# Kernel tuning notes

Hardware: AMD Instinct MI355X
Metric: run time of the kernel (lower is better)

## Reference

```python
import jax, jax.numpy as jnp
import numpy as np

N, E, G = 100000, 1600000, 1000
D_IN, D, L, C = 128, 300, 5, 10


def setup_inputs() -> dict:
    key = jax.random.key(0)
    ks = jax.random.split(key, 32)
    s = 0.05
    inp = {
        'x': jax.random.normal(ks[0], (N, D_IN), jnp.float32),
        'edge_index': jax.random.randint(ks[1], (2, E), 0, N, jnp.int64),
        'batch': jnp.sort(jax.random.randint(ks[2], (N,), 0, G, jnp.int64)),
        'enc_W': jax.random.normal(ks[3], (D_IN, D)) * s,
        'enc_b': jnp.zeros((D,)),
        'eps': jnp.zeros((L,)),
        'cW1': jax.random.normal(ks[4], (L, D, 2 * D)) * s,
        'cb1': jnp.zeros((L, 2 * D)),
        'cbn_s': jnp.ones((L, 2 * D)),
        'cbn_b': jnp.zeros((L, 2 * D)),
        'cW2': jax.random.normal(ks[5], (L, 2 * D, D)) * s,
        'cb2': jnp.zeros((L, D)),
        'bn_s': jnp.ones((L, D)),
        'bn_b': jnp.zeros((L, D)),
        'vn0': jnp.zeros((D,)),
        'vW1': jax.random.normal(ks[6], (L, D, 2 * D)) * s,
        'vb1': jnp.zeros((L, 2 * D)),
        'vbn1_s': jnp.ones((L, 2 * D)),
        'vbn1_b': jnp.zeros((L, 2 * D)),
        'vW2': jax.random.normal(ks[7], (L, 2 * D, D)) * s,
        'vb2': jnp.zeros((L, D)),
        'vbn2_s': jnp.ones((L, D)),
        'vbn2_b': jnp.zeros((L, D)),
        'gW1': jax.random.normal(ks[8], (D, 2 * D)) * s,
        'gb1': jnp.zeros((2 * D,)),
        'gbn_s': jnp.ones((2 * D,)),
        'gbn_b': jnp.zeros((2 * D,)),
        'gW2': jax.random.normal(ks[9], (2 * D, 1)) * s,
        'gb2': jnp.zeros((1,)),
        'pW': jax.random.normal(ks[10], (D, C)) * s,
        'pb': jnp.zeros((C,)),
    }
    return inp


def reference(x, enc_W, enc_b, eps, cW1, cb1, cbn_s, cbn_b, cW2, cb2,
              bn_s, bn_b, vn0, vW1, vb1, vbn1_s, vbn1_b, vW2, vb2,
              vbn2_s, vbn2_b, gW1, gb1, gbn_s, gbn_b, gW2, gb2, pW, pb,
              edge_index, batch):
    src, dst = edge_index[0], edge_index[1]
    n = x.shape[0]
    vn = jnp.broadcast_to(vn0, (G, D))  # virtualnode_embedding(zeros) -> row 0 per graph
    h_list = [x @ enc_W + enc_b]
    for l in range(L):
        hl = h_list[l] + vn[batch]  # virtual-node broadcast gather
        # GIN conv: MLP((1+eps)*h + sum_{j in N(i)} h_j)
        agg = jax.ops.segment_sum(hl[src], dst, num_segments=n)
        t = (1.0 + eps[l]) * hl + agg
        t = jax.nn.relu((t @ cW1[l] + cb1[l]) * cbn_s[l] + cbn_b[l])
        h = (t @ cW2[l] + cb2[l]) * bn_s[l] + bn_b[l]  # layer BN (eval, folded)
        if l < L - 1:
            h = jax.nn.relu(h)  # dropout is identity in eval
        # virtual-node update: global_add_pool + MLP
        vtmp = jax.ops.segment_sum(hl, batch, num_segments=G) + vn
        u = jax.nn.relu((vtmp @ vW1[l] + vb1[l]) * vbn1_s[l] + vbn1_b[l])
        vn = jax.nn.relu((u @ vW2[l] + vb2[l]) * vbn2_s[l] + vbn2_b[l])
        h_list.append(h)
    # JK = 'max' across all L+1 layer outputs
    nr = jnp.max(jnp.stack(h_list, axis=0), axis=0)  # [N, D]
    # GlobalAttention pooling: gate_nn -> per-graph segment softmax
    gate = (jax.nn.relu((nr @ gW1 + gb1) * gbn_s + gbn_b) @ gW2 + gb2)[:, 0]
    gmax = jax.ops.segment_max(gate, batch, num_segments=G)
    e = jnp.exp(gate - gmax[batch])
    denom = jax.ops.segment_sum(e, batch, num_segments=G)
    alpha = e / denom[batch]
    graph_rep = jax.ops.segment_sum(nr * alpha[:, None], batch, num_segments=G)
    return graph_rep @ pW + pb  # [G, C]
```

## Files before the change

### kernel.cpp

```cpp
#include <hip/hip_runtime.h>
#include <cstddef>

#define NGRAPH 1000
#define NEDGES 1600000
#define DD     300
#define DD2    600
#define DIN    128
#define NLAYER 5
#define NCLS   10
#define BR     32
#define BRM    32

#define NT2 38
#define NK2 10
#define NT3 19
#define NK3 19
#define WFRAG 1024
#define W1F_SZ (NT2*NK2*WFRAG)

typedef unsigned short u16;
typedef unsigned char  u8;
typedef unsigned int   u32;
typedef __attribute__((ext_vector_type(8))) short short8;
typedef __attribute__((ext_vector_type(4))) short short4v;
typedef __attribute__((ext_vector_type(4))) float f32x4;

__device__ __forceinline__ u16 f2bf(float f) {
    u32 u; __builtin_memcpy(&u, &f, 4);
    u = (u + 0x7FFFu + ((u >> 16) & 1u)) >> 16;
    return (u16)u;
}
__device__ __forceinline__ float bf2f(u16 h) {
    u32 u = ((u32)h) << 16;
    float f; __builtin_memcpy(&f, &u, 4); return f;
}

__device__ __forceinline__ float ld24(const u16* __restrict__ hi, const u8* __restrict__ lo,
                                      size_t idx) {
    u32 u = ((u32)hi[idx] << 16) | ((u32)lo[idx] << 8);
    float f; __builtin_memcpy(&f, &u, 4); return f;
}
__device__ __forceinline__ void st24(u16* __restrict__ hi, u8* __restrict__ lo,
                                     size_t idx, float f) {
    u32 u; __builtin_memcpy(&u, &f, 4);
    u32 r = u + 0x7Fu + ((u >> 8) & 1u);
    hi[idx] = (u16)(r >> 16); lo[idx] = (u8)(r >> 8);
}
__device__ __forceinline__ void ld24x4(const u16* __restrict__ hi, const u8* __restrict__ lo,
                                       size_t idx, float o[4]) {
    ushort4 h = *(const ushort4*)(hi + idx);
    uchar4  l = *(const uchar4*)(lo + idx);
    u32 u0 = ((u32)h.x << 16) | ((u32)l.x << 8);
    u32 u1 = ((u32)h.y << 16) | ((u32)l.y << 8);
    u32 u2 = ((u32)h.z << 16) | ((u32)l.z << 8);
    u32 u3 = ((u32)h.w << 16) | ((u32)l.w << 8);
    __builtin_memcpy(&o[0], &u0, 4); __builtin_memcpy(&o[1], &u1, 4);
    __builtin_memcpy(&o[2], &u2, 4); __builtin_memcpy(&o[3], &u3, 4);
}
__device__ __forceinline__ void st24x4(u16* __restrict__ hi, u8* __restrict__ lo,
                                       size_t idx, const float v[4]) {
    u32 u[4];
#pragma unroll
    for (int q = 0; q < 4; ++q) {
        u32 t; __builtin_memcpy(&t, &v[q], 4);
        u[q] = t + 0x7Fu + ((t >> 8) & 1u);
    }
    ushort4 h; h.x = (u16)(u[0] >> 16); h.y = (u16)(u[1] >> 16);
    h.z = (u16)(u[2] >> 16); h.w = (u16)(u[3] >> 16);
    uchar4 l8; l8.x = (u8)(u[0] >> 8); l8.y = (u8)(u[1] >> 8);
    l8.z = (u8)(u[2] >> 8); l8.w = (u8)(u[3] >> 8);
    *(ushort4*)(hi + idx) = h;
    *(uchar4*)(lo + idx) = l8;
}

__global__ void diag_kernel(float* __restrict__ out, int n, float val)
{
    int i = blockIdx.x * 256 + threadIdx.x;
    if (i < n) out[i] = val;
}

__global__ void vn_init_kernel(float* __restrict__ vn, const float* __restrict__ vn0)
{
    int idx = blockIdx.x * 256 + threadIdx.x;
    if (idx < NGRAPH * DD) vn[idx] = vn0[idx % DD];
}

__global__ void bconv_kernel(const int* __restrict__ braw, int n, int* __restrict__ b32)
{
    int i = blockIdx.x * 256 + threadIdx.x;
    if (i >= n) return;
    int fs = (braw[n - 1] == 0) ? 2 : 1;
    b32[i] = braw[(size_t)i * fs];
}

__global__ void packW_kernel(const float* __restrict__ W, int K, int N,
                             int nT, int nK, short* __restrict__ dst)
{
    int idx = blockIdx.x * 256 + threadIdx.x;
    int total = nT * nK * 64;
    if (idx >= total) return;
    int lane = idx & 63;
    int tk = idx >> 6;
    int nn = (tk / nK) * 16 + (lane & 15);
    int k0 = (tk % nK) * 32 + (lane >> 4) * 8;
    short* o = dst + ((size_t)tk << 10) + lane * 8;
#pragma unroll
    for (int j = 0; j < 8; ++j) {
        float v = (nn < N && (k0 + j) < K) ? W[(size_t)(k0 + j) * N + nn] : 0.f;
        u16 h = f2bf(v);
        o[j] = (short)h;
        o[512 + j] = (short)f2bf(v - bf2f(h));
    }
}

__global__ void deg_kernel(const int* __restrict__ ei, int fe, int E, int* __restrict__ deg)
{
    int e = blockIdx.x * 256 + threadIdx.x;
    if (e < E) atomicAdd(&deg[ei[(size_t)fe * (E + e)]], 1);
}

__global__ void scan_kernel(const int* __restrict__ deg, int* __restrict__ row_ptr, int n)
{
    __shared__ int sd[1024];
    int t = threadIdx.x;
    int C = (n + 1023) >> 10;
    int i0 = t * C, i1 = i0 + C; if (i1 > n) i1 = n; if (i0 > n) i0 = n;
    int s = 0;
    for (int i = i0; i < i1; ++i) s += deg[i];
    sd[t] = s;
    __syncthreads();
    for (int o = 1; o < 1024; o <<= 1) {
        int x = (t >= o) ? sd[t - o] : 0;
        __syncthreads();
        sd[t] += x;
        __syncthreads();
    }
    int run = (t == 0) ? 0 : sd[t - 1];
    for (int i = i0; i < i1; ++i) { row_ptr[i] = run; run += deg[i]; }
    if (t == 1023) row_ptr[n] = sd[1023];
}

__global__ void scatter_kernel(const int* __restrict__ ei, int fe, int E,
                               int* __restrict__ cursor, int* __restrict__ col_idx)
{
    int e = blockIdx.x * 256 + threadIdx.x;
    if (e < E) {
        int d = ei[(size_t)fe * (E + e)];
        int s = ei[(size_t)fe * e];
        int p = atomicAdd(&cursor[d], 1);
        col_idx[p] = s;
    }
}

__device__ __forceinline__ int lower_bound_i(const int* __restrict__ arr, int n, int key)
{
    int lo = 0, hi = n;
    while (lo < hi) {
        int mid = (lo + hi) >> 1;
        if (arr[mid] < key) lo = mid + 1; else hi = mid;
    }
    return lo;
}

__global__ void vtmp_kernel(const u16* __restrict__ hi, const u8* __restrict__ lo,
                            const int* __restrict__ batch, const float* __restrict__ vn,
                            float* __restrict__ vtmp, int n)
{
    int g = blockIdx.x, t = threadIdx.x;
    int l0 = lower_bound_i(batch, n, g);
    int h0 = lower_bound_i(batch, n, g + 1);
    if (t >= DD) return;
    float a0 = 0.f, a1 = 0.f, a2 = 0.f, a3 = 0.f;
    int i = l0;
    for (; i + 3 < h0; i += 4) {
        a0 += ld24(hi, lo, (size_t)(i + 0) * DD + t);
        a1 += ld24(hi, lo, (size_t)(i + 1) * DD + t);
        a2 += ld24(hi, lo, (size_t)(i + 2) * DD + t);
        a3 += ld24(hi, lo, (size_t)(i + 3) * DD + t);
    }
    for (; i < h0; ++i) a0 += ld24(hi, lo, (size_t)i * DD + t);
    vtmp[(size_t)g * DD + t] = ((a0 + a1) + (a2 + a3)) + vn[(size_t)g * DD + t];
}

__global__ void vn_mlp_kernel(const float* __restrict__ vtmp,
                              const float* __restrict__ W1, const float* __restrict__ b1,
                              const float* __restrict__ s1, const float* __restrict__ sb1,
                              const float* __restrict__ W2, const float* __restrict__ b2,
                              const float* __restrict__ s2, const float* __restrict__ sb2,
                              float* __restrict__ vn)
{
    __shared__ float vt[DD];
    __shared__ float us[DD2];
    int g = blockIdx.x, t = threadIdx.x;
    if (t < DD) vt[t] = vtmp[(size_t)g * DD + t];
    __syncthreads();
    for (int j = t; j < DD2; j += 512) {
        float acc = 0.f;
        for (int k = 0; k < DD; ++k) acc = fmaf(vt[k], W1[(size_t)k * DD2 + j], acc);
        us[j] = fmaxf(fmaf(acc + b1[j], s1[j], sb1[j]), 0.f);
    }
    __syncthreads();
    for (int j = t; j < DD; j += 512) {
        float acc = 0.f;
        for (int k = 0; k < DD2; ++k) acc = fmaf(us[k], W2[(size_t)k * DD + j], acc);
        vn[(size_t)g * DD + j] = fmaxf(fmaf(acc + b2[j], s2[j], sb2[j]), 0.f);
    }
}

__global__ __launch_bounds__(1024)
void encoder_kernel(const float* __restrict__ x, const float* __restrict__ W,
                    const float* __restrict__ b,
                    u16* __restrict__ Ahi, u8* __restrict__ Alo,
                    short* __restrict__ NRm, float* __restrict__ NRscale, int n)
{
    __shared__ float xs[BR][DIN];
    __shared__ float wmax[16][8];
    __shared__ float rowS[BR];
    const int tid = threadIdx.x;
    const int base = blockIdx.x * BR;
    for (int idx = tid; idx < BR * DIN; idx += 1024) {
        int r = idx >> 7, c = idx & 127;
        int node = base + r;
        xs[r][c] = (node < n) ? x[(size_t)node * DIN + c] : 0.f;
    }
    __syncthreads();
    const int rq = tid >> 8, ct = tid & 255;
    const int wid = tid >> 6, lane = tid & 63;
    const int j0 = ct; const bool has1 = ct < (DD - 256); const int j1 = ct + 256;
    float acc[8][2] = {};
    for (int k = 0; k < DIN; ++k) {
        const float* wr = W + (size_t)k * DD;
        float w0 = wr[j0], w1 = has1 ? wr[j1] : 0.f;
#pragma unroll
        for (int i = 0; i < 8; ++i) {
            float a = xs[rq * 8 + i][k];
            acc[i][0] = fmaf(a, w0, acc[i][0]);
            acc[i][1] = fmaf(a, w1, acc[i][1]);
        }
    }
    float bb0 = b[j0], bb1 = has1 ? b[j1] : 0.f;
    float v0[8], v1[8], lm[8];
#pragma unroll
    for (int i = 0; i < 8; ++i) {
        v0[i] = acc[i][0] + bb0;
        v1[i] = has1 ? (acc[i][1] + bb1) : 0.f;
        lm[i] = fmaxf(fabsf(v0[i]), fabsf(v1[i]));
    }
#pragma unroll
    for (int o = 32; o > 0; o >>= 1)
#pragma unroll
        for (int i = 0; i < 8; ++i) lm[i] = fmaxf(lm[i], __shfl_xor(lm[i], o));
    if (lane == 0)
#pragma unroll
        for (int i = 0; i < 8; ++i) wmax[wid][i] = lm[i];
    __syncthreads();
    if (ct < 8) {
        int r = rq * 8 + ct;
        float m = fmaxf(fmaxf(wmax[4 * rq][ct], wmax[4 * rq + 1][ct]),
                        fmaxf(wmax[4 * rq + 2][ct], wmax[4 * rq + 3][ct]));
        float S = fmaxf(m, 1e-30f) / 32767.f;
        rowS[r] = S;
        if (base + r < n) NRscale[base + r] = S;
    }
    __syncthreads();
#pragma unroll
    for (int i = 0; i < 8; ++i) {
        int r = rq * 8 + i;
        int node = base + r;
        if (node >= n) continue;
        float S = rowS[r];
        size_t idx = (size_t)node * DD + j0;
        st24(Ahi, Alo, idx, v0[i]);
        NRm[idx] = (short)rintf(v0[i] / S);
        if (has1) {
            st24(Ahi, Alo, idx + 256, v1[i]);
            NRm[idx + 256] = (short)rintf(v1[i] / S);
        }
    }
}

__global__ __launch_bounds__(256)
void agg_kernel(const u16* __restrict__ Phi, const u8* __restrict__ Plo,
                u16* __restrict__ Qhi, u8* __restrict__ Qlo,
                const int* __restrict__ row_ptr, const int* __restrict__ col_idx,
                const float* __restrict__ eps, int l, int n)
{
    int node = blockIdx.x * 4 + (threadIdx.x >> 6);
    int lane = threadIdx.x & 63;
    if (node >= n) return;
    const float ep = 1.0f + eps[l];
    const bool two = (lane < 11);
    float a0[4] = {0.f, 0.f, 0.f, 0.f}, a1[4] = {0.f, 0.f, 0.f, 0.f};
    int e0 = row_ptr[node], e1 = row_ptr[node + 1];
    for (int e = e0; e < e1; ++e) {
        int src = col_idx[e];
        size_t rb = (size_t)src * DD;
        float v[4];
        ld24x4(Phi, Plo, rb + lane * 4, v);
        a0[0] += v[0]; a0[1] += v[1]; a0[2] += v[2]; a0[3] += v[3];
        if (two) {
            ld24x4(Phi, Plo, rb + 256 + lane * 4, v);
            a1[0] += v[0]; a1[1] += v[1]; a1[2] += v[2]; a1[3] += v[3];
        }
    }
    size_t ob = (size_t)node * DD;
    float v[4], o[4];
    ld24x4(Phi, Plo, ob + lane * 4, v);
#pragma unroll
    for (int q = 0; q < 4; ++q) o[q] = fmaf(ep, v[q], a0[q]);
    st24x4(Qhi, Qlo, ob + lane * 4, o);
    if (two) {
        ld24x4(Phi, Plo, ob + 256 + lane * 4, v);
#pragma unroll
        for (int q = 0; q < 4; ++q) o[q] = fmaf(ep, v[q], a1[q]);
        st24x4(Qhi, Qlo, ob + 256 + lane * 4, o);
    }
}

__global__ __launch_bounds__(512)
void mlp_kernel(u16* __restrict__ Qhi, u8* __restrict__ Qlo,
                short* __restrict__ NRm, float* __restrict__ NRscale,
                const short* __restrict__ W1f, const float* __restrict__ b1,
                const float* __restrict__ s1, const float* __restrict__ sb1,
                const short* __restrict__ W2f, const float* __restrict__ b2,
                const float* __restrict__ s2, const float* __restrict__ sb2,
                int relu2, const float* __restrict__ vnp,
                const int* __restrict__ batch, int writeQ, int n)
{
    __shared__ char uni[78848];
    __shared__ float rowM[32], rowSo[32], rowSn[32];
    short* agh = (short*)uni;
    short* agl = (short*)(uni + 20992);
    short* tlh = (short*)uni;
    short* tll = (short*)(uni + 39424);
    float* outb = (float*)uni;

    const int tid = threadIdx.x;
    const int base = blockIdx.x * BRM;
    const int wv = tid >> 6, lane = tid & 63;
    const int cl = lane & 15, kq = lane >> 4, r0 = kq * 4;

    for (int idx = tid; idx < 32 * 80; idx += 512) {
        int r = idx / 80, c4 = (idx - r * 80) * 4;
        int node = base + r;
        float v[4] = {0.f, 0.f, 0.f, 0.f};
        if (c4 < DD && node < n) ld24x4(Qhi, Qlo, (size_t)node * DD + c4, v);
        short4v hh, ll;
#pragma unroll
        for (int q = 0; q < 4; ++q) {
            u16 h = f2bf(v[q]);
            hh[q] = (short)h;
            ll[q] = (short)f2bf(v[q] - bf2f(h));
        }
        *(short4v*)&agh[r * 328 + c4] = hh;
        *(short4v*)&agl[r * 328 + c4] = ll;
    }
    __syncthreads();

    {
        f32x4 acc[2][5];
#pragma unroll
        for (int s = 0; s < 2; ++s)
#pragma unroll
            for (int i = 0; i < 5; ++i) acc[s][i] = (f32x4){0.f, 0.f, 0.f, 0.f};
        const bool act5 = (wv + 32) < NT2;
        for (int ks = 0; ks < NK2; ++ks) {
            short8 bh[5], bl[5];
#pragma unroll
            for (int i = 0; i < 5; ++i) {
                int t = wv + 8 * i;
                if (i < 4 || act5) {
                    const short* bp = W1f + (((size_t)t * NK2 + ks) << 10) + lane * 8;
                    bh[i] = *(const short8*)bp;
                    bl[i] = *(const short8*)(bp + 512);
                }
            }
            short8 ah0 = *(const short8*)&agh[cl * 328 + kq * 8 + ks * 32];
            short8 al0 = *(const short8*)&agl[cl * 328 + kq * 8 + ks * 32];
            short8 ah1 = *(const short8*)&agh[(16 + cl) * 328 + kq * 8 + ks * 32];
            short8 al1 = *(const short8*)&agl[(16 + cl) * 328 + kq * 8 + ks * 32];
#pragma unroll
            for (int i = 0; i < 5; ++i)
                if (i < 4 || act5) {
                    acc[0][i] = __builtin_amdgcn_mfma_f32_16x16x32_bf16(ah0, bh[i], acc[0][i], 0, 0, 0);
                    acc[1][i] = __builtin_amdgcn_mfma_f32_16x16x32_bf16(ah1, bh[i], acc[1][i], 0, 0, 0);
                }
#pragma unroll
            for (int i = 0; i < 5; ++i)
                if (i < 4 || act5) {
                    acc[0][i] = __builtin_amdgcn_mfma_f32_16x16x32_bf16(ah0, bl[i], acc[0][i], 0, 0, 0);
                    acc[1][i] = __builtin_amdgcn_mfma_f32_16x16x32_bf16(ah1, bl[i], acc[1][i], 0, 0, 0);
                }
#pragma unroll
            for (int i = 0; i < 5; ++i)
                if (i < 4 || act5) {
                    acc[0][i] = __builtin_amdgcn_mfma_f32_16x16x32_bf16(al0, bh[i], acc[0][i], 0, 0, 0);
                    acc[1][i] = __builtin_amdgcn_mfma_f32_16x16x32_bf16(al1, bh[i], acc[1][i], 0, 0, 0);
                }
        }
        __syncthreads();
        if (tid < 256) {
            int r = tid >> 3, c = 600 + (tid & 7);
            tlh[r * 616 + c] = 0; tll[r * 616 + c] = 0;
        }
#pragma unroll
        for (int s = 0; s < 2; ++s)
#pragma unroll
            for (int i = 0; i < 5; ++i) {
                int t = wv + 8 * i;
                if (t >= NT2) continue;
                int cg = t * 16 + cl;
                if (cg < DD2) {
                    float bb = b1[cg], ss = s1[cg], cc = sb1[cg];
#pragma unroll
                    for (int r = 0; r < 4; ++r) {
                        float xv = fmaxf(fmaf(acc[s][i][r] + bb, ss, cc), 0.f);
                        u16 h = f2bf(xv);
                        tlh[(s * 16 + r0 + r) * 616 + cg] = (short)h;
                        tll[(s * 16 + r0 + r) * 616 + cg] = (short)f2bf(xv - bf2f(h));
                    }
                }
            }
    }
    __syncthreads();

    {
        f32x4 acc[2][3];
#pragma unroll
        for (int s = 0; s < 2; ++s)
#pragma unroll
            for (int i = 0; i < 3; ++i) acc[s][i] = (f32x4){0.f, 0.f, 0.f, 0.f};
        const bool act3 = (wv + 16) < NT3;
        for (int ks = 0; ks < NK3; ++ks) {
            short8 bh[3], bl[3];
#pragma unroll
            for (int i = 0; i < 3; ++i) {
                int t = wv + 8 * i;
                if (i < 2 || act3) {
                    const short* bp = W2f + (((size_t)t * NK3 + ks) << 10) + lane * 8;
                    bh[i] = *(const short8*)bp;
                    bl[i] = *(const short8*)(bp + 512);
                }
            }
            short8 ah0 = *(const short8*)&tlh[cl * 616 + kq * 8 + ks * 32];
            short8 al0 = *(const short8*)&tll[cl * 616 + kq * 8 + ks * 32];
            short8 ah1 = *(const short8*)&tlh[(16 + cl) * 616 + kq * 8 + ks * 32];
            short8 al1 = *(const short8*)&tll[(16 + cl) * 616 + kq * 8 + ks * 32];
#pragma unroll
            for (int i = 0; i < 3; ++i)
                if (i < 2 || act3) {
                    acc[0][i] = __builtin_amdgcn_mfma_f32_16x16x32_bf16(ah0, bh[i], acc[0][i], 0, 0, 0);
                    acc[1][i] = __builtin_amdgcn_mfma_f32_16x16x32_bf16(ah1, bh[i], acc[1][i], 0, 0, 0);
                }
#pragma unroll
            for (int i = 0; i < 3; ++i)
                if (i < 2 || act3) {
                    acc[0][i] = __builtin_amdgcn_mfma_f32_16x16x32_bf16(ah0, bl[i], acc[0][i], 0, 0, 0);
                    acc[1][i] = __builtin_amdgcn_mfma_f32_16x16x32_bf16(ah1, bl[i], acc[1][i], 0, 0, 0);
                }
#pragma unroll
            for (int i = 0; i < 3; ++i)
                if (i < 2 || act3) {
                    acc[0][i] = __builtin_amdgcn_mfma_f32_16x16x32_bf16(al0, bh[i], acc[0][i], 0, 0, 0);
                    acc[1][i] = __builtin_amdgcn_mfma_f32_16x16x32_bf16(al1, bh[i], acc[1][i], 0, 0, 0);
                }
        }
        __syncthreads();
#pragma unroll
        for (int s = 0; s < 2; ++s)
#pragma unroll
            for (int i = 0; i < 3; ++i) {
                int t = wv + 8 * i;
                if (t >= NT3) continue;
                int cg = t * 16 + cl;
#pragma unroll
                for (int r = 0; r < 4; ++r) outb[(s * 16 + r0 + r) * 304 + cg] = acc[s][i][r];
            }
    }
    __syncthreads();

    {
        const int rr = tid >> 4;
        const int qq = tid & 15;
        float lm = 0.f;
        for (int c = qq; c < DD; c += 16) {
            float v = fmaf(outb[rr * 304 + c] + b2[c], s2[c], sb2[c]);
            if (relu2) v = fmaxf(v, 0.f);
            outb[rr * 304 + c] = v;
            lm = fmaxf(lm, fabsf(v));
        }
#pragma unroll
        for (int o = 8; o > 0; o >>= 1) lm = fmaxf(lm, __shfl_xor(lm, o));
        if (qq == 0) rowM[rr] = lm;
    }
    __syncthreads();
    if (tid < 32) {
        int node = base + tid;
        float oS = (node < n) ? NRscale[node] : 0.f;
        float newM = fmaxf(rowM[tid], oS * 32767.f);
        float nS = fmaxf(newM, 1e-30f) / 32767.f;
        rowSo[tid] = oS; rowSn[tid] = nS;
        if (node < n) NRscale[node] = nS;
    }
    __syncthreads();
    for (int idx = tid; idx < 32 * 75; idx += 512) {
        int r = idx / 75, c = (idx - r * 75) * 4;
        int node = base + r;
        if (node >= n) continue;
        float oS = rowSo[r], inv = 1.0f / rowSn[r];
        size_t gidx = (size_t)node * DD + c;
        float h0 = outb[r * 304 + c + 0];
        float h1 = outb[r * 304 + c + 1];
        float h2 = outb[r * 304 + c + 2];
        float h3 = outb[r * 304 + c + 3];
        if (writeQ) {
            float hl[4];
            if (vnp) {
                const float* vrow = vnp + (size_t)batch[node] * DD;
                float4 vv = *(const float4*)(vrow + c);
                hl[0] = h0 + vv.x; hl[1] = h1 + vv.y; hl[2] = h2 + vv.z; hl[3] = h3 + vv.w;
            } else {
                hl[0] = h0; hl[1] = h1; hl[2] = h2; hl[3] = h3;
            }
            st24x4(Qhi, Qlo, gidx, hl);
        }
        short4v old = *(const short4v*)&NRm[gidx];
        short4v nw;
        nw[0] = (short)rintf(fmaxf((float)old[0] * oS, h0) * inv);
        nw[1] = (short)rintf(fmaxf((float)old[1] * oS, h1) * inv);
        nw[2] = (short)rintf(fmaxf((float)old[2] * oS, h2) * inv);
        nw[3] = (short)rintf(fmaxf((float)old[3] * oS, h3) * inv);
        *(short4v*)&NRm[gidx] = nw;
    }
}

__global__ __launch_bounds__(512)
void gate_kernel(const short* __restrict__ NRm, const float* __restrict__ NRscale,
                 const short* __restrict__ W1f, const float* __restrict__ b1,
                 const float* __restrict__ s1, const float* __restrict__ sb1,
                 const float* __restrict__ W2, const float* __restrict__ b2,
                 float* __restrict__ gate, int n)
{
    __shared__ char uni[78336];
    __shared__ float sc[32];
    short* nbh = (short*)uni;
    short* nbl = (short*)(uni + 20992);
    float* tlf = (float*)uni;

    const int tid = threadIdx.x;
    const int base = blockIdx.x * BRM;
    const int wv = tid >> 6, lane = tid & 63;
    const int cl = lane & 15, kq = lane >> 4, r0 = kq * 4;

    if (tid < 32) {
        int node = base + tid;
        sc[tid] = (node < n) ? NRscale[node] : 0.f;
    }
    __syncthreads();
    for (int idx = tid; idx < 32 * 80; idx += 512) {
        int r = idx / 80, c4 = (idx - r * 80) * 4;
        int node = base + r;
        float v[4] = {0.f, 0.f, 0.f, 0.f};
        if (c4 < DD && node < n) {
            short4v m4 = *(const short4v*)&NRm[(size_t)node * DD + c4];
            float s = sc[r];
            v[0] = (float)m4[0] * s; v[1] = (float)m4[1] * s;
            v[2] = (float)m4[2] * s; v[3] = (float)m4[3] * s;
        }
        short4v hh, ll;
#pragma unroll
        for (int q = 0; q < 4; ++q) {
            u16 h = f2bf(v[q]);
            hh[q] = (short)h;
            ll[q] = (short)f2bf(v[q] - bf2f(h));
        }
        *(short4v*)&nbh[r * 328 + c4] = hh;
        *(short4v*)&nbl[r * 328 + c4] = ll;
    }
    __syncthreads();

    {
        f32x4 acc[2][5];
#pragma unroll
        for (int s = 0; s < 2; ++s)
#pragma unroll
            for (int i = 0; i < 5; ++i) acc[s][i] = (f32x4){0.f, 0.f, 0.f, 0.f};
        const bool act5 = (wv + 32) < NT2;
        for (int ks = 0; ks < NK2; ++ks) {
            short8 bh[5], bl[5];
#pragma unroll
            for (int i = 0; i < 5; ++i) {
                int t = wv + 8 * i;
                if (i < 4 || act5) {
                    const short* bp = W1f + (((size_t)t * NK2 + ks) << 10) + lane * 8;
                    bh[i] = *(const short8*)bp;
                    bl[i] = *(const short8*)(bp + 512);
                }
            }
            short8 ah0 = *(const short8*)&nbh[cl * 328 + kq * 8 + ks * 32];
            short8 al0 = *(const short8*)&nbl[cl * 328 + kq * 8 + ks * 32];
            short8 ah1 = *(const short8*)&nbh[(16 + cl) * 328 + kq * 8 + ks * 32];
            short8 al1 = *(const short8*)&nbl[(16 + cl) * 328 + kq * 8 + ks * 32];
#pragma unroll
            for (int i = 0; i < 5; ++i)
                if (i < 4 || act5) {
                    acc[0][i] = __builtin_amdgcn_mfma_f32_16x16x32_bf16(ah0, bh[i], acc[0][i], 0, 0, 0);
                    acc[1][i] = __builtin_amdgcn_mfma_f32_16x16x32_bf16(ah1, bh[i], acc[1][i], 0, 0, 0);
                }
#pragma unroll
            for (int i = 0; i < 5; ++i)
                if (i < 4 || act5) {
                    acc[0][i] = __builtin_amdgcn_mfma_f32_16x16x32_bf16(ah0, bl[i], acc[0][i], 0, 0, 0);
                    acc[1][i] = __builtin_amdgcn_mfma_f32_16x16x32_bf16(ah1, bl[i], acc[1][i], 0, 0, 0);
                }
#pragma unroll
            for (int i = 0; i < 5; ++i)
                if (i < 4 || act5) {
                    acc[0][i] = __builtin_amdgcn_mfma_f32_16x16x32_bf16(al0, bh[i], acc[0][i], 0, 0, 0);
                    acc[1][i] = __builtin_amdgcn_mfma_f32_16x16x32_bf16(al1, bh[i], acc[1][i], 0, 0, 0);
                }
        }
        __syncthreads();
#pragma unroll
        for (int s = 0; s < 2; ++s)
#pragma unroll
            for (int i = 0; i < 5; ++i) {
                int t = wv + 8 * i;
                if (t >= NT2) continue;
                int cg = t * 16 + cl;
                if (cg < DD2) {
                    float bb = b1[cg], ss = s1[cg], cc = sb1[cg];
#pragma unroll
                    for (int r = 0; r < 4; ++r)
                        tlf[(s * 16 + r0 + r) * 612 + cg] = fmaxf(fmaf(acc[s][i][r] + bb, ss, cc), 0.f);
                }
            }
    }
    __syncthreads();

    {
        const int wave = tid >> 6, ln = tid & 63;
#pragma unroll
        for (int rr = 0; rr < 4; ++rr) {
            int r = wave * 4 + rr;
            int node = base + r;
            float acc = 0.f;
            for (int j = ln; j < DD2; j += 64) acc = fmaf(tlf[r * 612 + j], W2[j], acc);
#pragma unroll
            for (int o = 32; o > 0; o >>= 1) acc += __shfl_down(acc, o);
            if (ln == 0 && node < n) gate[node] = acc + b2[0];
        }
    }
}

__global__ void attn_pool_kernel(const float* __restrict__ gate,
                                 const short* __restrict__ NRm, const float* __restrict__ NRscale,
                                 const int* __restrict__ batch, float* __restrict__ rep, int n)
{
    __shared__ float red[320];
    __shared__ float bc[2];
    int g = blockIdx.x, t = threadIdx.x;
    int l0 = lower_bound_i(batch, n, g);
    int h0 = lower_bound_i(batch, n, g + 1);
    if (l0 >= h0) { if (t < DD) rep[(size_t)g * DD + t] = 0.f; return; }

    float m = -3.4e38f;
    for (int i = l0 + t; i < h0; i += 320) m = fmaxf(m, gate[i]);
    red[t] = m;
    __syncthreads();
    if (t < 64) {
        float mm = red[t];
        for (int s2 = t + 64; s2 < 320; s2 += 64) mm = fmaxf(mm, red[s2]);
#pragma unroll
        for (int o = 32; o > 0; o >>= 1) mm = fmaxf(mm, __shfl_down(mm, o));
        if (t == 0) bc[0] = mm;
    }
    __syncthreads();
    float gmax = bc[0];

    float ssum = 0.f;
    for (int i = l0 + t; i < h0; i += 320) ssum += expf(gate[i] - gmax);
    __syncthreads();
    red[t] = ssum;
    __syncthreads();
    if (t < 64) {
        float mm = red[t];
        for (int s2 = t + 64; s2 < 320; s2 += 64) mm += red[s2];
#pragma unroll
        for (int o = 32; o > 0; o >>= 1) mm += __shfl_down(mm, o);
        if (t == 0) bc[1] = mm;
    }
    __syncthreads();
    float inv = 1.0f / bc[1];

    if (t < DD) {
        float acc = 0.f;
        for (int i = l0; i < h0; ++i) {
            float w = expf(gate[i] - gmax) * inv;
            acc = fmaf(w, (float)NRm[(size_t)i * DD + t] * NRscale[i], acc);
        }
        rep[(size_t)g * DD + t] = acc;
    }
}

__global__ void final_kernel(const float* __restrict__ rep, const float* __restrict__ pW,
                             const float* __restrict__ pb, float* __restrict__ out)
{
    int g = blockIdx.x, lane = threadIdx.x;
    float a[NCLS] = {};
    for (int d = lane; d < DD; d += 64) {
        float r = rep[(size_t)g * DD + d];
#pragma unroll
        for (int c = 0; c < NCLS; ++c) a[c] = fmaf(r, pW[d * NCLS + c], a[c]);
    }
#pragma unroll
    for (int c = 0; c < NCLS; ++c) {
#pragma unroll
        for (int o = 32; o > 0; o >>= 1) a[c] += __shfl_down(a[c], o);
    }
    if (lane == 0) {
#pragma unroll
        for (int c = 0; c < NCLS; ++c) out[g * NCLS + c] = a[c] + pb[c];
    }
}

extern "C" void kernel_launch(void* const* d_in, const int* in_sizes, int n_in,
                              void* d_out, int out_size, void* d_ws, size_t ws_size,
                              hipStream_t stream)
{
    (void)n_in;
    const float* x      = (const float*)d_in[0];
    const int*   ei     = (const int*)d_in[1];
    const int*   braw   = (const int*)d_in[2];
    const float* enc_W  = (const float*)d_in[3];
    const float* enc_b  = (const float*)d_in[4];
    const float* eps    = (const float*)d_in[5];
    const float* cW1    = (const float*)d_in[6];
    const float* cb1    = (const float*)d_in[7];
    const float* cbn_s  = (const float*)d_in[8];
    const float* cbn_b  = (const float*)d_in[9];
    const float* cW2    = (const float*)d_in[10];
    const float* cb2    = (const float*)d_in[11];
    const float* bn_s   = (const float*)d_in[12];
    const float* bn_b   = (const float*)d_in[13];
    const float* vn0    = (const float*)d_in[14];
    const float* vW1    = (const float*)d_in[15];
    const float* vb1    = (const float*)d_in[16];
    const float* vbn1_s = (const float*)d_in[17];
    const float* vbn1_b = (const float*)d_in[18];
    const float* vW2    = (const float*)d_in[19];
    const float* vb2    = (const float*)d_in[20];
    const float* vbn2_s = (const float*)d_in[21];
    const float* vbn2_b = (const float*)d_in[22];
    const float* gW1    = (const float*)d_in[23];
    const float* gb1    = (const float*)d_in[24];
    const float* gbn_s  = (const float*)d_in[25];
    const float* gbn_b  = (const float*)d_in[26];
    const float* gW2    = (const float*)d_in[27];
    const float* gb2    = (const float*)d_in[28];
    const float* pW     = (const float*)d_in[29];
    const float* pb     = (const float*)d_in[30];
    float* out = (float*)d_out;

    const int N = in_sizes[0] / DIN;
    const int E = NEDGES;
    int fe = in_sizes[1] / (2 * E);
    if (fe < 1) fe = 1; if (fe > 2) fe = 2;

    char* wsp = (char*)d_ws;
    size_t off = 0;
    auto carve = [&](size_t nbytes) -> void* {
        void* p = (void*)(wsp + off);
        off += ((nbytes + 255) / 256) * 256;
        return p;
    };
    u16*   Ahi     = (u16*)  carve((size_t)N * DD * 2);
    u8*    Alo     = (u8*)   carve((size_t)N * DD);
    u16*   Bhi     = (u16*)  carve((size_t)N * DD * 2);
    u8*    Blo     = (u8*)   carve((size_t)N * DD);
    short* NRm     = (short*)carve((size_t)N * DD * 2);
    float* NRscale = (float*)carve((size_t)N * 4);
    float* vnBuf   = (float*)carve((size_t)NGRAPH * DD * 4);
    float* vtmpBuf = (float*)carve((size_t)NGRAPH * DD * 4);
    float* repBuf  = (float*)carve((size_t)NGRAPH * DD * 4);
    float* gateBuf = (float*)carve((size_t)N * 4);
    int*   batch32 = (int*)  carve((size_t)N * 4);
    int*   row_ptr = (int*)  carve(((size_t)N + 1) * 4);
    int*   cursor  = (int*)  carve((size_t)N * 4);
    int*   col_idx = (int*)  carve((size_t)E * 4);
    short* W1f     = (short*)carve((size_t)NLAYER * W1F_SZ * 2);
    short* W2f     = (short*)carve((size_t)NLAYER * W1F_SZ * 2);
    short* gW1f    = (short*)carve((size_t)W1F_SZ * 2);

    if (off > ws_size) {
        diag_kernel<<<(out_size + 255) / 256, 256, 0, stream>>>(out, out_size, (float)ws_size);
        return;
    }

    const int pkBlocks = (NT2 * NK2 * 64 + 255) / 256;
    for (int l = 0; l < NLAYER; ++l) {
        packW_kernel<<<pkBlocks, 256, 0, stream>>>(cW1 + (size_t)l * DD * DD2, DD, DD2,
                                                   NT2, NK2, W1f + (size_t)l * W1F_SZ);
        packW_kernel<<<pkBlocks, 256, 0, stream>>>(cW2 + (size_t)l * DD2 * DD, DD2, DD,
                                                   NT3, NK3, W2f + (size_t)l * W1F_SZ);
    }
    packW_kernel<<<pkBlocks, 256, 0, stream>>>(gW1, DD, DD2, NT2, NK2, gW1f);

    bconv_kernel<<<(N + 255) / 256, 256, 0, stream>>>(braw, N, batch32);

    (void)hipMemsetAsync(cursor, 0, (size_t)N * 4, stream);
    deg_kernel<<<(E + 255) / 256, 256, 0, stream>>>(ei, fe, E, cursor);
    scan_kernel<<<1, 1024, 0, stream>>>(cursor, row_ptr, N);
    (void)hipMemcpyAsync(cursor, row_ptr, (size_t)N * 4, hipMemcpyDeviceToDevice, stream);
    scatter_kernel<<<(E + 255) / 256, 256, 0, stream>>>(ei, fe, E, cursor, col_idx);

    vn_init_kernel<<<(NGRAPH * DD + 255) / 256, 256, 0, stream>>>(vnBuf, vn0);

    const int nblk32 = (N + BR - 1) / BR;
    const int nblkM  = (N + BRM - 1) / BRM;
    const int nblk4  = (N + 3) / 4;

    encoder_kernel<<<nblk32, 1024, 0, stream>>>(x, enc_W, enc_b, Ahi, Alo, NRm, NRscale, N);

    u16 *Phi = Ahi, *Qhi = Bhi; u8 *Plo = Alo, *Qlo = Blo;
    for (int l = 0; l < NLAYER; ++l) {
        const bool hasVn = (l < NLAYER - 1);
        if (hasVn)
            vtmp_kernel<<<NGRAPH, 320, 0, stream>>>(Phi, Plo, batch32, vnBuf, vtmpBuf, N);
        agg_kernel<<<nblk4, 256, 0, stream>>>(Phi, Plo, Qhi, Qlo, row_ptr, col_idx, eps, l, N);
        if (hasVn)
            vn_mlp_kernel<<<NGRAPH, 512, 0, stream>>>(
                vtmpBuf,
                vW1 + (size_t)l * DD * DD2, vb1 + (size_t)l * DD2,
                vbn1_s + (size_t)l * DD2, vbn1_b + (size_t)l * DD2,
                vW2 + (size_t)l * DD2 * DD, vb2 + (size_t)l * DD,
                vbn2_s + (size_t)l * DD, vbn2_b + (size_t)l * DD,
                vnBuf);
        mlp_kernel<<<nblkM, 512, 0, stream>>>(
            Qhi, Qlo, NRm, NRscale,
            W1f + (size_t)l * W1F_SZ, cb1 + (size_t)l * DD2,
            cbn_s + (size_t)l * DD2, cbn_b + (size_t)l * DD2,
            W2f + (size_t)l * W1F_SZ, cb2 + (size_t)l * DD,
            bn_s + (size_t)l * DD, bn_b + (size_t)l * DD,
            hasVn ? 1 : 0,
            hasVn ? vnBuf : (const float*)nullptr, batch32,
            hasVn ? 1 : 0, N);
        u16* th = Phi; Phi = Qhi; Qhi = th;
        u8*  tb = Plo; Plo = Qlo; Qlo = tb;
    }

    gate_kernel<<<nblkM, 512, 0, stream>>>(NRm, NRscale, gW1f, gb1, gbn_s, gbn_b,
                                           gW2, gb2, gateBuf, N);
    attn_pool_kernel<<<NGRAPH, 320, 0, stream>>>(gateBuf, NRm, NRscale, batch32, repBuf, N);
    final_kernel<<<NGRAPH, 64, 0, stream>>>(repBuf, pW, pb, out);
}
```

Before: 3.985 ms.

## Fuse GIN neighbor aggregation into the MLP kernel via shared memory

Removes the separate aggregation kernel. The fused gin_kernel gathers neighbor rows from CSR, applies (1+eps)*h plus the sum per row, and writes the split bf16 hi/lo values straight into the MLP's shared-memory staging tile. This avoids writing the aggregated tensor to global memory and reading it back, and saves one launch per layer. In exchange, the irregular gather now runs inside a 512-thread block with large shared-memory use, where each wave serially handles 4 rows. That can lower occupancy and latency hiding for the memory-bound gather.

```diff
diff --git a/kernel.cpp b/kernel.cpp
--- a/kernel.cpp
+++ b/kernel.cpp
@@ -279,47 +279,12 @@
     }
 }
 
-__global__ __launch_bounds__(256)
-void agg_kernel(const u16* __restrict__ Phi, const u8* __restrict__ Plo,
+__global__ __launch_bounds__(512)
+void gin_kernel(const u16* __restrict__ Phi, const u8* __restrict__ Plo,
                 u16* __restrict__ Qhi, u8* __restrict__ Qlo,
+                short* __restrict__ NRm, float* __restrict__ NRscale,
                 const int* __restrict__ row_ptr, const int* __restrict__ col_idx,
-                const float* __restrict__ eps, int l, int n)
-{
-    int node = blockIdx.x * 4 + (threadIdx.x >> 6);
-    int lane = threadIdx.x & 63;
-    if (node >= n) return;
-    const float ep = 1.0f + eps[l];
-    const bool two = (lane < 11);
-    float a0[4] = {0.f, 0.f, 0.f, 0.f}, a1[4] = {0.f, 0.f, 0.f, 0.f};
-    int e0 = row_ptr[node], e1 = row_ptr[node + 1];
-    for (int e = e0; e < e1; ++e) {
-        int src = col_idx[e];
-        size_t rb = (size_t)src * DD;
-        float v[4];
-        ld24x4(Phi, Plo, rb + lane * 4, v);
-        a0[0] += v[0]; a0[1] += v[1]; a0[2] += v[2]; a0[3] += v[3];
-        if (two) {
-            ld24x4(Phi, Plo, rb + 256 + lane * 4, v);
-            a1[0] += v[0]; a1[1] += v[1]; a1[2] += v[2]; a1[3] += v[3];
-        }
-    }
-    size_t ob = (size_t)node * DD;
-    float v[4], o[4];
-    ld24x4(Phi, Plo, ob + lane * 4, v);
-#pragma unroll
-    for (int q = 0; q < 4; ++q) o[q] = fmaf(ep, v[q], a0[q]);
-    st24x4(Qhi, Qlo, ob + lane * 4, o);
-    if (two) {
-        ld24x4(Phi, Plo, ob + 256 + lane * 4, v);
-#pragma unroll
-        for (int q = 0; q < 4; ++q) o[q] = fmaf(ep, v[q], a1[q]);
-        st24x4(Qhi, Qlo, ob + 256 + lane * 4, o);
-    }
-}
-
-__global__ __launch_bounds__(512)
-void mlp_kernel(u16* __restrict__ Qhi, u8* __restrict__ Qlo,
-                short* __restrict__ NRm, float* __restrict__ NRscale,
+                const float* __restrict__ eps, int l,
                 const short* __restrict__ W1f, const float* __restrict__ b1,
                 const float* __restrict__ s1, const float* __restrict__ sb1,
                 const short* __restrict__ W2f, const float* __restrict__ b2,
@@ -340,20 +305,62 @@
     const int wv = tid >> 6, lane = tid & 63;
     const int cl = lane & 15, kq = lane >> 4, r0 = kq * 4;
 
-    for (int idx = tid; idx < 32 * 80; idx += 512) {
-        int r = idx / 80, c4 = (idx - r * 80) * 4;
-        int node = base + r;
-        float v[4] = {0.f, 0.f, 0.f, 0.f};
-        if (c4 < DD && node < n) ld24x4(Qhi, Qlo, (size_t)node * DD + c4, v);
-        short4v hh, ll;
-#pragma unroll
-        for (int q = 0; q < 4; ++q) {
-            u16 h = f2bf(v[q]);
-            hh[q] = (short)h;
-            ll[q] = (short)f2bf(v[q] - bf2f(h));
-        }
-        *(short4v*)&agh[r * 328 + c4] = hh;
-        *(short4v*)&agl[r * 328 + c4] = ll;
+    {
+        const float ep = 1.0f + eps[l];
+        const bool two = (lane < 11);
+        const bool zpad = (lane >= 11 && lane < 16);
+#pragma unroll
+        for (int rr = 0; rr < 4; ++rr) {
+            int r = wv * 4 + rr;
+            int node = base + r;
+            float o0[4] = {0.f, 0.f, 0.f, 0.f}, o1[4] = {0.f, 0.f, 0.f, 0.f};
+            if (node < n) {
+                int e0 = row_ptr[node], e1 = row_ptr[node + 1];
+                for (int e = e0; e < e1; ++e) {
+                    int src = col_idx[e];
+                    size_t rb = (size_t)src * DD;
+                    float v[4];
+                    ld24x4(Phi, Plo, rb + lane * 4, v);
+                    o0[0] += v[0]; o0[1] += v[1]; o0[2] += v[2]; o0[3] += v[3];
+                    if (two) {
+                        ld24x4(Phi, Plo, rb + 256 + lane * 4, v);
+                        o1[0] += v[0]; o1[1] += v[1]; o1[2] += v[2]; o1[3] += v[3];
+                    }
+                }
+                float v[4];
+                ld24x4(Phi, Plo, (size_t)node * DD + lane * 4, v);
+#pragma unroll
+                for (int q = 0; q < 4; ++q) o0[q] = fmaf(ep, v[q], o0[q]);
+                if (two) {
+                    ld24x4(Phi, Plo, (size_t)node * DD + 256 + lane * 4, v);
+#pragma unroll
+                    for (int q = 0; q < 4; ++q) o1[q] = fmaf(ep, v[q], o1[q]);
+                }
+            }
+            {
+                short4v hh, ll;
+#pragma unroll
+                for (int q = 0; q < 4; ++q) {
+                    u16 h = f2bf(o0[q]);
+                    hh[q] = (short)h;
+                    ll[q] = (short)f2bf(o0[q] - bf2f(h));
+                }
+                *(short4v*)&agh[r * 328 + lane * 4] = hh;
+                *(short4v*)&agl[r * 328 + lane * 4] = ll;
+            }
+            if (two || zpad) {
+                short4v hh, ll;
+#pragma unroll
+                for (int q = 0; q < 4; ++q) {
+                    float val = two ? o1[q] : 0.f;
+                    u16 h = f2bf(val);
+                    hh[q] = (short)h;
+                    ll[q] = (short)f2bf(val - bf2f(h));
+                }
+                *(short4v*)&agh[r * 328 + 256 + lane * 4] = hh;
+                *(short4v*)&agl[r * 328 + 256 + lane * 4] = ll;
+            }
+        }
     }
     __syncthreads();
 
@@ -818,7 +825,6 @@
 
     const int nblk32 = (N + BR - 1) / BR;
     const int nblkM  = (N + BRM - 1) / BRM;
-    const int nblk4  = (N + 3) / 4;
 
     encoder_kernel<<<nblk32, 1024, 0, stream>>>(x, enc_W, enc_b, Ahi, Alo, NRm, NRscale, N);
 
@@ -827,7 +833,6 @@
         const bool hasVn = (l < NLAYER - 1);
         if (hasVn)
             vtmp_kernel<<<NGRAPH, 320, 0, stream>>>(Phi, Plo, batch32, vnBuf, vtmpBuf, N);
-        agg_kernel<<<nblk4, 256, 0, stream>>>(Phi, Plo, Qhi, Qlo, row_ptr, col_idx, eps, l, N);
         if (hasVn)
             vn_mlp_kernel<<<NGRAPH, 512, 0, stream>>>(
                 vtmpBuf,
@@ -836,8 +841,9 @@
                 vW2 + (size_t)l * DD2 * DD, vb2 + (size_t)l * DD,
                 vbn2_s + (size_t)l * DD, vbn2_b + (size_t)l * DD,
                 vnBuf);
-        mlp_kernel<<<nblkM, 512, 0, stream>>>(
-            Qhi, Qlo, NRm, NRscale,
+        gin_kernel<<<nblkM, 512, 0, stream>>>(
+            Phi, Plo, Qhi, Qlo, NRm, NRscale,
+            row_ptr, col_idx, eps, l,
             W1f + (size_t)l * W1F_SZ, cb1 + (size_t)l * DD2,
             cbn_s + (size_t)l * DD2, cbn_b + (size_t)l * DD2,
             W2f + (size_t)l * W1F_SZ, cb2 + (size_t)l * DD,
```

Measured after the change: 4.541 ms. +14.0%, slower.
